# Kernel tuning notes

Hardware: AMD Instinct MI355X
Metric: run time of the kernel (lower is better)

## Reference

```python
import jax, jax.numpy as jnp
import numpy as np

N_NODES = 50000
N_EDGES = 800000
IN_DIM, HID, OUT_DIM = 32, 96, 1
NEG_SLOPE = 0.2


def _glorot(key, shape):
    fan_in, fan_out = shape[0], shape[-1]
    lim = float(np.sqrt(6.0 / (fan_in + fan_out)))
    return jax.random.uniform(key, shape, jnp.float32, -lim, lim)


def setup_inputs() -> dict:
    key = jax.random.key(0)
    ks = jax.random.split(key, 20)
    inp = {
        "x": jax.random.normal(ks[0], (N_NODES, IN_DIM), jnp.float32),
        "edge_index": jax.random.randint(ks[1], (2, N_EDGES), 0, N_NODES, jnp.int64),
        "edge_weight": jax.random.uniform(ks[2], (N_EDGES,), jnp.float32),
    }
    dims = [(IN_DIM, HID), (HID, HID), (HID, HID), (HID, OUT_DIM)]
    names = ["0", "1", "2", "f"]
    k = 3
    for nm, (di, do) in zip(names, dims):
        inp["W" + nm] = _glorot(ks[k], (di, do)); k += 1
        inp["as" + nm] = _glorot(ks[k], (1, do))[0]; k += 1
        inp["ad" + nm] = _glorot(ks[k], (1, do))[0]; k += 1
        inp["b" + nm] = jnp.zeros((do,), jnp.float32)
    return inp


def _gat_conv(x, src, dst, n, W, a_s, a_d, b):
    # h: [N, out]; per-node attention logits, gathered per edge
    h = x @ W
    es = h @ a_s  # [N]
    ed = h @ a_d  # [N]
    e = jax.nn.leaky_relu(es[src] + ed[dst], NEG_SLOPE)  # [E]
    m = jax.ops.segment_max(e, dst, num_segments=n)  # segment-softmax (stable)
    ex = jnp.exp(e - m[dst])
    s = jax.ops.segment_sum(ex, dst, num_segments=n)
    alpha = ex / s[dst]  # every node has a self loop -> s > 0
    out = jax.ops.segment_sum(alpha[:, None] * h[src], dst, num_segments=n)
    return out + b


def reference(x, edge_index, edge_weight, W0, as0, ad0, b0, W1, as1, ad1, b1,
              W2, as2, ad2, b2, Wf, asf, adf, bf):
    # edge_weight is ignored: PyG GATConv with edge_dim=None drops edge_attr.
    n = x.shape[0]
    loops = jnp.arange(n, dtype=edge_index.dtype)
    src = jnp.concatenate([edge_index[0], loops])  # add_self_loops=True
    dst = jnp.concatenate([edge_index[1], loops])

    # dropout is identity in eval mode
    for (W, a_s, a_d, b) in [(W0, as0, ad0, b0), (W1, as1, ad1, b1), (W2, as2, ad2, b2)]:
        residual = x
        x = _gat_conv(x, src, dst, n, W, a_s, a_d, b)
        if x.shape == residual.shape:
            x = x + residual
        x = jax.nn.relu(x)
    return _gat_conv(x, src, dst, n, Wf, asf, adf, bf)
```

## Files before the change

kernel.cpp:

```cpp
#include <hip/hip_runtime.h>
#include <hip/hip_fp16.h>
#include <math.h>

#define N_NODES 50000
#define N_EDGES 800000
#define E_TOT   (N_EDGES + N_NODES)
#define IN_DIM  32
#define HID     96
#define NEG_SLOPE 0.2f
#define BUCKET  48
#define G_PAD   50
#define NBINS   196
#define BCAP    5120
#define GC_STRIDE 64
#define FILL_EPT 16
#define FILL_NB ((N_EDGES + 256 * FILL_EPT - 1) / (256 * FILL_EPT))
#define AGG_BLOCKS (N_NODES / 16)
#define PREP_BLOCKS ((N_NODES * 32) / 256)
#define WT_BLOCKS (((HID * HID) + 255) / 256)

typedef _Float16 half8v __attribute__((ext_vector_type(8)));
typedef float    float4v __attribute__((ext_vector_type(4)));

static inline int cdiv(long long a, int b) { return (int)((a + b - 1) / b); }

__device__ __forceinline__ int clamp_src(int s) {
    return (int)min((unsigned)s, (unsigned)(N_NODES - 1));
}

__device__ __forceinline__ float lrelu_exp(float v) {
    v = v > 0.f ? v : NEG_SLOPE * v;
    return __expf(v);
}

__device__ __forceinline__ void mfma_tile_epilogue(
    const __half* s_x , __half* s_t ,
    const __half* __restrict__ wt, const float* __restrict__ a_s,
    const float* __restrict__ a_d, __half* __restrict__ h,
    float* __restrict__ es, float* __restrict__ ed, int m0, int lane) {
    int col = lane & 15, quad = lane >> 4;
    const __half* arow = s_x + col * 104 + quad * 8;
    const __half* brow = wt + (size_t)col * 96 + quad * 8;

    float ps0 = 0.f, ps1 = 0.f, ps2 = 0.f, ps3 = 0.f;
    float pd0 = 0.f, pd1 = 0.f, pd2 = 0.f, pd3 = 0.f;
    #pragma unroll
    for (int p = 0; p < 2; ++p) {
        float4v acc[3];
        #pragma unroll
        for (int t = 0; t < 3; ++t) acc[t] = (float4v){0.f, 0.f, 0.f, 0.f};
        #pragma unroll
        for (int ks = 0; ks < 3; ++ks) {
            half8v afrag = *(const half8v*)(arow + ks * 32);
            #pragma unroll
            for (int t = 0; t < 3; ++t) {
                half8v bfrag = *(const half8v*)(brow + (size_t)(p * 3 + t) * 16 * 96 + ks * 32);
                acc[t] = __builtin_amdgcn_mfma_f32_16x16x32_f16(afrag, bfrag, acc[t], 0, 0, 0);
            }
        }
        #pragma unroll
        for (int t = 0; t < 3; ++t) {
            int ch = (p * 3 + t) * 16 + col;
            float sa = a_s[ch], sd = a_d[ch];
            float v0 = acc[t][0], v1 = acc[t][1], v2 = acc[t][2], v3 = acc[t][3];
            int r0 = quad * 4;
            s_t[(r0 + 0) * 104 + ch] = __float2half(v0);
            s_t[(r0 + 1) * 104 + ch] = __float2half(v1);
            s_t[(r0 + 2) * 104 + ch] = __float2half(v2);
            s_t[(r0 + 3) * 104 + ch] = __float2half(v3);
            ps0 += v0 * sa; ps1 += v1 * sa; ps2 += v2 * sa; ps3 += v3 * sa;
            pd0 += v0 * sd; pd1 += v1 * sd; pd2 += v2 * sd; pd3 += v3 * sd;
        }
    }
    #pragma unroll
    for (int o = 1; o < 16; o <<= 1) {
        ps0 += __shfl_xor(ps0, o); ps1 += __shfl_xor(ps1, o);
        ps2 += __shfl_xor(ps2, o); ps3 += __shfl_xor(ps3, o);
        pd0 += __shfl_xor(pd0, o); pd1 += __shfl_xor(pd1, o);
        pd2 += __shfl_xor(pd2, o); pd3 += __shfl_xor(pd3, o);
    }
    if (col == 0) {
        int nb = m0 + quad * 4;
        es[nb] = ps0; es[nb + 1] = ps1; es[nb + 2] = ps2; es[nb + 3] = ps3;
        ed[nb] = pd0; ed[nb + 1] = pd1; ed[nb + 2] = pd2; ed[nb + 3] = pd3;
    }
    {
        int trow = lane >> 2, q = lane & 3;
        const uint4* sr = (const uint4*)(s_t + trow * 104);
        uint4* H8 = (uint4*)h;
        size_t rb = (size_t)(m0 + trow) * 12;
        H8[rb + q]     = sr[q];
        H8[rb + q + 4] = sr[q + 4];
        H8[rb + q + 8] = sr[q + 8];
    }
}

__global__ __launch_bounds__(256) void build_prep_kernel(
    const int* __restrict__ ei, unsigned* __restrict__ gcnt,
    unsigned* __restrict__ ebuf,
    const float* __restrict__ x, const float* __restrict__ W0,
    const float* __restrict__ as0, const float* __restrict__ ad0,
    __half* __restrict__ xh, float* __restrict__ es, float* __restrict__ ed,
    const float* __restrict__ W1, const float* __restrict__ W2,
    __half* __restrict__ WT1, __half* __restrict__ WT2) {
    int b = blockIdx.x;
    if (b < FILL_NB) {
        __shared__ unsigned lcnt[256];
        __shared__ unsigned lbase[256];
        int tid = threadIdx.x;
        lcnt[tid] = 0u;
        __syncthreads();
        int e0 = (b * 256 + tid) * FILL_EPT;
        bool val = e0 < N_EDGES;
        unsigned pk[FILL_EPT];
        unsigned short rank[FILL_EPT];
        if (val) {
            #pragma unroll
            for (int q = 0; q < FILL_EPT / 4; ++q) {
                int4 d4 = *(const int4*)(ei + N_EDGES + e0 + q * 4);
                int4 s4 = *(const int4*)(ei + e0 + q * 4);
                int dd[4] = {d4.x, d4.y, d4.z, d4.w};
                int ss[4] = {s4.x, s4.y, s4.z, s4.w};
                #pragma unroll
                for (int k = 0; k < 4; ++k) {
                    int d = clamp_src(dd[k]);
                    int bin = d >> 8;
                    pk[q * 4 + k] = (unsigned)clamp_src(ss[k]) | ((unsigned)(d & 255) << 16)
                                  | ((unsigned)bin << 24);
                    rank[q * 4 + k] = (unsigned short)atomicAdd(&lcnt[bin], 1u);
                }
            }
        }
        __syncthreads();
        if (tid < NBINS) {
            unsigned c = lcnt[tid];
            lbase[tid] = c ? atomicAdd(gcnt + (size_t)tid * GC_STRIDE, c) : 0u;
        }
        __syncthreads();
        if (val) {
            #pragma unroll
            for (int k = 0; k < FILL_EPT; ++k) {
                unsigned bin = pk[k] >> 24;
                unsigned pos = lbase[bin] + rank[k];
                if (pos < BCAP) ebuf[(size_t)bin * BCAP + pos] = pk[k];
            }
        }
        return;
    }
    b -= FILL_NB;
    if (b >= PREP_BLOCKS) {
        int i = (b - PREP_BLOCKS) * 256 + threadIdx.x;
        if (i < HID * HID) {
            int n = i / HID, k = i - n * HID;
            WT1[i] = __float2half(W1[k * HID + n]);
            WT2[i] = __float2half(W2[k * HID + n]);
        }
        return;
    }
    __shared__ float s_us[32], s_ud[32];
    if (threadIdx.x < 64) {
        int k = threadIdx.x & 31;
        int sel = threadIdx.x >> 5;
        const float* a = sel ? ad0 : as0;
        float acc = 0.f;
        #pragma unroll 8
        for (int c = 0; c < HID; ++c) acc += W0[k * HID + c] * a[c];
        if (sel) s_ud[k] = acc; else s_us[k] = acc;
    }
    __syncthreads();
    int idx = b * 256 + threadIdx.x;
    int node = idx >> 5;
    int k = threadIdx.x & 31;
    float xv = x[(size_t)node * 32 + k];
    float xnb = __shfl_xor(xv, 1);
    if ((k & 1) == 0) {
        __half2 h2v = __floats2half2_rn(xv, xnb);
        ((__half2*)xh)[((size_t)node * 32 + k) >> 1] = h2v;
    }
    float ps = xv * s_us[k], pd = xv * s_ud[k];
    #pragma unroll
    for (int o = 16; o; o >>= 1) {
        ps += __shfl_xor(ps, o);
        pd += __shfl_xor(pd, o);
    }
    if (k == 0) { es[node] = ps; ed[node] = pd; }
}

__global__ __launch_bounds__(256) void bucket_build_kernel(
    const unsigned* __restrict__ gcnt, const unsigned* __restrict__ ebuf,
    unsigned* __restrict__ cnt, unsigned short* __restrict__ srcs) {
    __shared__ unsigned short lsr[256][BUCKET];
    __shared__ unsigned lct[256];
    int bin = blockIdx.x, tid = threadIdx.x;
    int nb = bin * 256 + tid;
    lct[tid] = 1u;
    lsr[tid][0] = (unsigned short)min(nb, N_NODES - 1);
    __syncthreads();
    unsigned ec = min(gcnt[(size_t)bin * GC_STRIDE], (unsigned)BCAP);
    for (unsigned j = tid; j < ec; j += 256) {
        unsigned pkv = ebuf[(size_t)bin * BCAP + j];
        unsigned dloc = (pkv >> 16) & 255u;
        unsigned pos = atomicAdd(&lct[dloc], 1u);
        if (pos < BUCKET) lsr[dloc][pos] = (unsigned short)(pkv & 0xFFFFu);
    }
    __syncthreads();
    if (nb < N_NODES) cnt[nb] = min(lct[tid], (unsigned)BUCKET);
    const uint4* ls4 = (const uint4*)&lsr[0][0];
    uint4* gs4 = (uint4*)(srcs + (size_t)bin * 256 * BUCKET);
    for (int i = tid; i < 256 * (BUCKET / 8); i += 256) {
        int node = i / (BUCKET / 8);
        if (bin * 256 + node < N_NODES) gs4[i] = ls4[i];
    }
}

__global__ __launch_bounds__(256) void aggregate32_kernel(
    const unsigned* __restrict__ cnt, const unsigned short* __restrict__ srcs,
    const float* __restrict__ es, const float* __restrict__ ed,
    const __half* __restrict__ xh,
    const float* __restrict__ W0, const float* __restrict__ b0,
    __half* __restrict__ x16a,
    const __half* __restrict__ wt1, const float* __restrict__ as1,
    const float* __restrict__ ad1, __half* __restrict__ hA,
    float* __restrict__ es2, float* __restrict__ ed2) {
    __shared__ uint2 sh[4][4][G_PAD];
    __shared__ float s_ag[16][33];
    __shared__ float4 s_w0[32][24];
    __shared__ __align__(16) __half s_x[16 * 104];
    __shared__ __align__(16) __half s_t[16 * 104];
    const float4* W4g = (const float4*)W0;
    for (int i = threadIdx.x; i < 32 * 24; i += 256)
        s_w0[i / 24][i % 24] = W4g[i];

    int lane = threadIdx.x & 63;
    int wv = threadIdx.x >> 6;
    int g = lane >> 4, lin = lane & 15;
    int node = blockIdx.x * 16 + wv * 4 + g;
    size_t row = (size_t)node * BUCKET;
    int deg = min((int)cnt[node], BUCKET);
    float edv = ed[node];

    float lsum;
    {
        int jA = lin, jB = lin + 16, jC = lin + 32;
        bool bA = jA < deg, bB = jB < deg, bC = jC < deg;
        int sA = clamp_src((int)srcs[row + (bA ? jA : 0)]);
        int sB = clamp_src((int)srcs[row + (bB ? jB : 0)]);
        int sC = clamp_src((int)srcs[row + (bC ? jC : 0)]);
        float gA = es[sA], gB = es[sB], gC = es[sC];
        float eA = bA ? lrelu_exp(gA + edv) : 0.f;
        float eB = bB ? lrelu_exp(gB + edv) : 0.f;
        float eC = bC ? lrelu_exp(gC + edv) : 0.f;
        uint2 pA; pA.x = (unsigned)sA; pA.y = __float_as_uint(eA);
        uint2 pB; pB.x = (unsigned)sB; pB.y = __float_as_uint(eB);
        uint2 pC; pC.x = (unsigned)sC; pC.y = __float_as_uint(eC);
        if (bA) sh[wv][g][jA] = pA;
        if (bB) sh[wv][g][jB] = pB;
        if (bC) sh[wv][g][jC] = pC;
        lsum = eA + eB + eC;
    }
    float4 acc = {0.f, 0.f, 0.f, 0.f};
    const uint2* x2 = (const uint2*)xh;
    int h8sel = lin >> 3;
    int c = lin & 7;

    int j = 0;
    for (; j + 8 <= deg; j += 8) {
        uint2 p0 = sh[wv][g][j + h8sel];
        uint2 p1 = sh[wv][g][j + 2 + h8sel];
        uint2 p2 = sh[wv][g][j + 4 + h8sel];
        uint2 p3 = sh[wv][g][j + 6 + h8sel];
        uint2 q0 = x2[(size_t)p0.x * 8 + c];
        uint2 q1 = x2[(size_t)p1.x * 8 + c];
        uint2 q2 = x2[(size_t)p2.x * 8 + c];
        uint2 q3 = x2[(size_t)p3.x * 8 + c];
        float e0 = __uint_as_float(p0.y), e1 = __uint_as_float(p1.y);
        float e2 = __uint_as_float(p2.y), e3 = __uint_as_float(p3.y);
        float2 f00 = __half22float2(*(__half2*)&q0.x), f01 = __half22float2(*(__half2*)&q0.y);
        float2 f10 = __half22float2(*(__half2*)&q1.x), f11 = __half22float2(*(__half2*)&q1.y);
        float2 f20 = __half22float2(*(__half2*)&q2.x), f21 = __half22float2(*(__half2*)&q2.y);
        float2 f30 = __half22float2(*(__half2*)&q3.x), f31 = __half22float2(*(__half2*)&q3.y);
        acc.x += e0 * f00.x + e1 * f10.x + e2 * f20.x + e3 * f30.x;
        acc.y += e0 * f00.y + e1 * f10.y + e2 * f20.y + e3 * f30.y;
        acc.z += e0 * f01.x + e1 * f11.x + e2 * f21.x + e3 * f31.x;
        acc.w += e0 * f01.y + e1 * f11.y + e2 * f21.y + e3 * f31.y;
    }
    for (; j + 4 <= deg; j += 4) {
        uint2 p0 = sh[wv][g][j + h8sel];
        uint2 p1 = sh[wv][g][j + 2 + h8sel];
        uint2 q0 = x2[(size_t)p0.x * 8 + c];
        uint2 q1 = x2[(size_t)p1.x * 8 + c];
        float e0 = __uint_as_float(p0.y), e1 = __uint_as_float(p1.y);
        float2 f00 = __half22float2(*(__half2*)&q0.x), f01 = __half22float2(*(__half2*)&q0.y);
        float2 f10 = __half22float2(*(__half2*)&q1.x), f11 = __half22float2(*(__half2*)&q1.y);
        acc.x += e0 * f00.x + e1 * f10.x; acc.y += e0 * f00.y + e1 * f10.y;
        acc.z += e0 * f01.x + e1 * f11.x; acc.w += e0 * f01.y + e1 * f11.y;
    }
    for (; j < deg; j += 2) {
        int idx = j + h8sel;
        if (idx < deg) {
            uint2 p = sh[wv][g][idx];
            uint2 q = x2[(size_t)p.x * 8 + c];
            float e = __uint_as_float(p.y);
            float2 f0 = __half22float2(*(__half2*)&q.x);
            float2 f1 = __half22float2(*(__half2*)&q.y);
            acc.x += e * f0.x; acc.y += e * f0.y;
            acc.z += e * f1.x; acc.w += e * f1.y;
        }
    }
    #pragma unroll
    for (int o = 1; o < 16; o <<= 1) lsum += __shfl_xor(lsum, o);
    acc.x += __shfl_xor(acc.x, 8);
    acc.y += __shfl_xor(acc.y, 8);
    acc.z += __shfl_xor(acc.z, 8);
    acc.w += __shfl_xor(acc.w, 8);
    if (lin < 8) {
        float inv = 1.f / lsum;
        int n = wv * 4 + g;
        s_ag[n][lin * 4 + 0] = acc.x * inv;
        s_ag[n][lin * 4 + 1] = acc.y * inv;
        s_ag[n][lin * 4 + 2] = acc.z * inv;
        s_ag[n][lin * 4 + 3] = acc.w * inv;
    }
    __syncthreads();
    int t = threadIdx.x;
    if (t < 192) {
        int n = t / 12, c8 = t - n * 12;
        int onode = blockIdx.x * 16 + n;
        float4 a0v = {0.f, 0.f, 0.f, 0.f}, a1v = {0.f, 0.f, 0.f, 0.f};
        #pragma unroll 8
        for (int k = 0; k < 32; ++k) {
            float a = s_ag[n][k];
            float4 w0 = s_w0[k][c8 * 2], w1 = s_w0[k][c8 * 2 + 1];
            a0v.x += a * w0.x; a0v.y += a * w0.y; a0v.z += a * w0.z; a0v.w += a * w0.w;
            a1v.x += a * w1.x; a1v.y += a * w1.y; a1v.z += a * w1.z; a1v.w += a * w1.w;
        }
        float4 bb0 = ((const float4*)b0)[c8 * 2], bb1 = ((const float4*)b0)[c8 * 2 + 1];
        float v0 = fmaxf(a0v.x + bb0.x, 0.f), v1 = fmaxf(a0v.y + bb0.y, 0.f);
        float v2 = fmaxf(a0v.z + bb0.z, 0.f), v3 = fmaxf(a0v.w + bb0.w, 0.f);
        float v4 = fmaxf(a1v.x + bb1.x, 0.f), v5 = fmaxf(a1v.y + bb1.y, 0.f);
        float v6 = fmaxf(a1v.z + bb1.z, 0.f), v7 = fmaxf(a1v.w + bb1.w, 0.f);
        __half2 q0 = __floats2half2_rn(v0, v1), q1 = __floats2half2_rn(v2, v3);
        __half2 q2 = __floats2half2_rn(v4, v5), q3 = __floats2half2_rn(v6, v7);
        uint4 st; st.x = *(unsigned*)&q0; st.y = *(unsigned*)&q1;
        st.z = *(unsigned*)&q2; st.w = *(unsigned*)&q3;
        ((uint4*)x16a)[(size_t)onode * 12 + c8] = st;
        *(uint4*)(s_x + n * 104 + c8 * 8) = st;
    }
    __syncthreads();
    if (threadIdx.x < 64)
        mfma_tile_epilogue(s_x, s_t, wt1, as1, ad1, hA, es2, ed2,
                           blockIdx.x * 16, lane);
}

__global__ __launch_bounds__(256) void aggregate96_kernel(
    const unsigned* __restrict__ cnt, const unsigned short* __restrict__ srcs,
    const float* __restrict__ es, const float* __restrict__ ed,
    const __half* __restrict__ h, const float* __restrict__ b,
    const __half* __restrict__ res16, __half* __restrict__ out16,
    const float* __restrict__ Wf, float* __restrict__ hfin,
    const __half* __restrict__ wtproj, const float* __restrict__ as_n,
    const float* __restrict__ ad_n, __half* __restrict__ h_out,
    float* __restrict__ es_n, float* __restrict__ ed_n) {
    __shared__ uint2 sh[4][4][G_PAD];
    __shared__ __align__(16) __half s_x[16 * 104];
    __shared__ __align__(16) __half s_t[16 * 104];
    int lane = threadIdx.x & 63;
    int wv = threadIdx.x >> 6;
    int g = lane >> 4, lin = lane & 15;
    int node = blockIdx.x * 16 + wv * 4 + g;
    size_t row = (size_t)node * BUCKET;
    int deg = min((int)cnt[node], BUCKET);
    float edv = ed[node];

    float lsum;
    {
        int jA = lin, jB = lin + 16, jC = lin + 32;
        bool bA = jA < deg, bB = jB < deg, bC = jC < deg;
        int sA = clamp_src((int)srcs[row + (bA ? jA : 0)]);
        int sB = clamp_src((int)srcs[row + (bB ? jB : 0)]);
        int sC = clamp_src((int)srcs[row + (bC ? jC : 0)]);
        float gA = es[sA], gB = es[sB], gC = es[sC];
        float eA = bA ? lrelu_exp(gA + edv) : 0.f;
        float eB = bB ? lrelu_exp(gB + edv) : 0.f;
        float eC = bC ? lrelu_exp(gC + edv) : 0.f;
        uint2 pA; pA.x = (unsigned)sA; pA.y = __float_as_uint(eA);
        uint2 pB; pB.x = (unsigned)sB; pB.y = __float_as_uint(eB);
        uint2 pC; pC.x = (unsigned)sC; pC.y = __float_as_uint(eC);
        if (bA) sh[wv][g][jA] = pA;
        if (bB) sh[wv][g][jB] = pB;
        if (bC) sh[wv][g][jC] = pC;
        lsum = eA + eB + eC;
    }
    float a0 = 0.f, a1 = 0.f, a2 = 0.f, a3 = 0.f, a4 = 0.f, a5 = 0.f, a6 = 0.f, a7 = 0.f;
    const uint4* h8 = (const uint4*)h;
    bool act = (lin < 12);

    int j = 0;
    for (; j + 4 <= deg; j += 4) {
        uint2 p0 = sh[wv][g][j];
        uint2 p1 = sh[wv][g][j + 1];
        uint2 p2 = sh[wv][g][j + 2];
        uint2 p3 = sh[wv][g][j + 3];
        if (act) {
            uint4 q0 = h8[(size_t)p0.x * 12 + lin];
            uint4 q1 = h8[(size_t)p1.x * 12 + lin];
            uint4 q2 = h8[(size_t)p2.x * 12 + lin];
            uint4 q3 = h8[(size_t)p3.x * 12 + lin];
            float e0 = __uint_as_float(p0.y), e1 = __uint_as_float(p1.y);
            float e2 = __uint_as_float(p2.y), e3 = __uint_as_float(p3.y);
            float2 fa0 = __half22float2(*(__half2*)&q0.x), fa1 = __half22float2(*(__half2*)&q0.y);
            float2 fa2 = __half22float2(*(__half2*)&q0.z), fa3 = __half22float2(*(__half2*)&q0.w);
            float2 fb0 = __half22float2(*(__half2*)&q1.x), fb1 = __half22float2(*(__half2*)&q1.y);
            float2 fb2 = __half22float2(*(__half2*)&q1.z), fb3 = __half22float2(*(__half2*)&q1.w);
            float2 fc0 = __half22float2(*(__half2*)&q2.x), fc1 = __half22float2(*(__half2*)&q2.y);
            float2 fc2 = __half22float2(*(__half2*)&q2.z), fc3 = __half22float2(*(__half2*)&q2.w);
            float2 fd0 = __half22float2(*(__half2*)&q3.x), fd1 = __half22float2(*(__half2*)&q3.y);
            float2 fd2 = __half22float2(*(__half2*)&q3.z), fd3 = __half22float2(*(__half2*)&q3.w);
            a0 += e0 * fa0.x + e1 * fb0.x + e2 * fc0.x + e3 * fd0.x;
            a1 += e0 * fa0.y + e1 * fb0.y + e2 * fc0.y + e3 * fd0.y;
            a2 += e0 * fa1.x + e1 * fb1.x + e2 * fc1.x + e3 * fd1.x;
            a3 += e0 * fa1.y + e1 * fb1.y + e2 * fc1.y + e3 * fd1.y;
            a4 += e0 * fa2.x + e1 * fb2.x + e2 * fc2.x + e3 * fd2.x;
            a5 += e0 * fa2.y + e1 * fb2.y + e2 * fc2.y + e3 * fd2.y;
            a6 += e0 * fa3.x + e1 * fb3.x + e2 * fc3.x + e3 * fd3.x;
            a7 += e0 * fa3.y + e1 * fb3.y + e2 * fc3.y + e3 * fd3.y;
        }
    }
    for (; j < deg; ++j) {
        uint2 p = sh[wv][g][j];
        if (act) {
            uint4 q = h8[(size_t)p.x * 12 + lin];
            float e = __uint_as_float(p.y);
            float2 f0 = __half22float2(*(__half2*)&q.x);
            float2 f1 = __half22float2(*(__half2*)&q.y);
            float2 f2 = __half22float2(*(__half2*)&q.z);
            float2 f3 = __half22float2(*(__half2*)&q.w);
            a0 += e * f0.x; a1 += e * f0.y;
            a2 += e * f1.x; a3 += e * f1.y;
            a4 += e * f2.x; a5 += e * f2.y;
            a6 += e * f3.x; a7 += e * f3.y;
        }
    }
    #pragma unroll
    for (int o = 1; o < 16; o <<= 1) lsum += __shfl_xor(lsum, o);

    float pfin = 0.f;
    if (act) {
        float inv = 1.f / lsum;
        const float4* b4 = (const float4*)b;
        float4 bb0 = b4[lin * 2], bb1 = b4[lin * 2 + 1];
        float v0 = a0 * inv + bb0.x, v1 = a1 * inv + bb0.y;
        float v2 = a2 * inv + bb0.z, v3 = a3 * inv + bb0.w;
        float v4 = a4 * inv + bb1.x, v5 = a5 * inv + bb1.y;
        float v6 = a6 * inv + bb1.z, v7 = a7 * inv + bb1.w;
        if (res16) {
            uint4 rr = ((const uint4*)res16)[(size_t)node * 12 + lin];
            float2 r0 = __half22float2(*(__half2*)&rr.x);
            float2 r1 = __half22float2(*(__half2*)&rr.y);
            float2 r2 = __half22float2(*(__half2*)&rr.z);
            float2 r3 = __half22float2(*(__half2*)&rr.w);
            v0 += r0.x; v1 += r0.y; v2 += r1.x; v3 += r1.y;
            v4 += r2.x; v5 += r2.y; v6 += r3.x; v7 += r3.y;
        }
        v0 = fmaxf(v0, 0.f); v1 = fmaxf(v1, 0.f); v2 = fmaxf(v2, 0.f); v3 = fmaxf(v3, 0.f);
        v4 = fmaxf(v4, 0.f); v5 = fmaxf(v5, 0.f); v6 = fmaxf(v6, 0.f); v7 = fmaxf(v7, 0.f);
        __half2 q0 = __floats2half2_rn(v0, v1), q1 = __floats2half2_rn(v2, v3);
        __half2 q2 = __floats2half2_rn(v4, v5), q3 = __floats2half2_rn(v6, v7);
        uint4 st; st.x = *(unsigned*)&q0; st.y = *(unsigned*)&q1;
        st.z = *(unsigned*)&q2; st.w = *(unsigned*)&q3;
        if (out16) ((uint4*)out16)[(size_t)node * 12 + lin] = st;
        if (wtproj) {
            int n = wv * 4 + g;
            *(uint4*)(s_x + n * 104 + lin * 8) = st;
        }
        if (hfin) {
            const float4* w4 = (const float4*)Wf;
            float4 wf0 = w4[lin * 2], wf1 = w4[lin * 2 + 1];
            pfin = v0 * wf0.x + v1 * wf0.y + v2 * wf0.z + v3 * wf0.w
                 + v4 * wf1.x + v5 * wf1.y + v6 * wf1.z + v7 * wf1.w;
        }
    }
    if (hfin) {
        #pragma unroll
        for (int o = 1; o < 16; o <<= 1) pfin += __shfl_xor(pfin, o);
        if (lin == 0) hfin[node] = pfin;
    }
    if (wtproj) {
        __syncthreads();
        if (threadIdx.x < 64)
            mfma_tile_epilogue(s_x, s_t, wtproj, as_n, ad_n, h_out, es_n, ed_n,
                               blockIdx.x * 16, lane);
    }
}

__global__ __launch_bounds__(256) void aggregate1_kernel(
    const unsigned* __restrict__ cnt, const unsigned short* __restrict__ srcs,
    const float* __restrict__ hfin, const float* __restrict__ asf,
    const float* __restrict__ adf, const float* __restrict__ bf,
    float* __restrict__ out) {
    int lane = threadIdx.x & 63;
    int wv = threadIdx.x >> 6;
    int g = lane >> 4, lin = lane & 15;
    int node = blockIdx.x * 16 + wv * 4 + g;
    size_t row = (size_t)node * BUCKET;
    int deg = min((int)cnt[node], BUCKET);
    float as0 = asf[0], ad0 = adf[0];
    float edv = hfin[node] * ad0;

    float lsum = 0.f, acc = 0.f;
    for (int base = 0; base < deg; base += 32) {
        int i0 = base + lin * 2;
        if (i0 < deg) {
            unsigned sv = *(const unsigned*)(srcs + row + i0);
            int s0 = clamp_src((int)(sv & 0xFFFFu));
            int s1 = clamp_src((int)(sv >> 16));
            float h0 = hfin[s0], h1 = hfin[s1];
            float v0 = as0 * h0 + edv;
            v0 = v0 > 0.f ? v0 : NEG_SLOPE * v0;
            float ex0 = __expf(v0);
            lsum += ex0; acc += ex0 * h0;
            if (i0 + 1 < deg) {
                float v1 = as0 * h1 + edv;
                v1 = v1 > 0.f ? v1 : NEG_SLOPE * v1;
                float ex1 = __expf(v1);
                lsum += ex1; acc += ex1 * h1;
            }
        }
    }
    #pragma unroll
    for (int o = 1; o < 16; o <<= 1) {
        lsum += __shfl_xor(lsum, o);
        acc  += __shfl_xor(acc, o);
    }
    if (lin == 0) out[node] = acc / lsum + bf[0];
}


extern "C" void kernel_launch(void* const* d_in, const int* in_sizes, int n_in,
                              void* d_out, int out_size, void* d_ws, size_t ws_size,
                              hipStream_t stream) {
    const float* x  = (const float*)d_in[0];
    const int*   ei = (const int*)d_in[1];
    const float* W0 = (const float*)d_in[3];
    const float* as0 = (const float*)d_in[4];
    const float* ad0 = (const float*)d_in[5];
    const float* b0 = (const float*)d_in[6];
    const float* W1 = (const float*)d_in[7];
    const float* as1 = (const float*)d_in[8];
    const float* ad1 = (const float*)d_in[9];
    const float* b1 = (const float*)d_in[10];
    const float* W2 = (const float*)d_in[11];
    const float* as2 = (const float*)d_in[12];
    const float* ad2 = (const float*)d_in[13];
    const float* b2 = (const float*)d_in[14];
    const float* Wf = (const float*)d_in[15];
    const float* asf = (const float*)d_in[16];
    const float* adf = (const float*)d_in[17];
    const float* bf = (const float*)d_in[18];

    float* out = (float*)d_out;

    float* Hf = (float*)d_ws;
    __half* H16A = (__half*)Hf;
    __half* H16B = H16A + (size_t)N_NODES * HID;
    float* ES = Hf + (long long)N_NODES * HID;
    float* ED = ES + N_NODES;
    unsigned* CNT = (unsigned*)(ED + N_NODES);
    unsigned short* SRCS = (unsigned short*)(CNT + N_NODES);
    __half* X16A = (__half*)(SRCS + (size_t)N_NODES * BUCKET);
    __half* X16B = X16A + (size_t)N_NODES * HID;
    __half* WT1 = X16B + (size_t)N_NODES * HID;
    __half* WT2 = WT1 + HID * HID;
    float* HFIN = (float*)(WT2 + HID * HID);
    __half* XH = (__half*)(HFIN + N_NODES);
    unsigned* GCNT = (unsigned*)(XH + (size_t)N_NODES * 32);
    unsigned* EBUF = GCNT + (size_t)NBINS * GC_STRIDE;
    float* ES2 = (float*)(EBUF + (size_t)NBINS * BCAP);
    float* ED2 = ES2 + N_NODES;

    hipMemsetAsync(GCNT, 0, (size_t)NBINS * GC_STRIDE * sizeof(unsigned), stream);
    build_prep_kernel<<<FILL_NB + PREP_BLOCKS + WT_BLOCKS, 256, 0, stream>>>(
        ei, GCNT, EBUF, x, W0, as0, ad0, XH, ES, ED, W1, W2, WT1, WT2);
    bucket_build_kernel<<<NBINS, 256, 0, stream>>>(GCNT, EBUF, CNT, SRCS);

    aggregate32_kernel<<<AGG_BLOCKS, 256, 0, stream>>>(
        CNT, SRCS, ES, ED, XH, W0, b0, X16A, WT1, as1, ad1, H16A, ES2, ED2);

    aggregate96_kernel<<<AGG_BLOCKS, 256, 0, stream>>>(
        CNT, SRCS, ES2, ED2, H16A, b1, X16A, X16B, nullptr, nullptr,
        WT2, as2, ad2, H16B, ES, ED);

    aggregate96_kernel<<<AGG_BLOCKS, 256, 0, stream>>>(
        CNT, SRCS, ES, ED, H16B, b2, X16B, nullptr, Wf, HFIN,
        nullptr, nullptr, nullptr, nullptr, nullptr, nullptr);

    aggregate1_kernel<<<AGG_BLOCKS, 256, 0, stream>>>(CNT, SRCS, HFIN, asf, adf, bf, out);
}
```

Measured before the change: 231.7 us.

## Sort nodes by degree within bins to balance aggregation wavefronts

The bucket build now computes a per-bin counting sort of nodes by in-degree and writes a permutation array. All aggregation kernels process nodes in that permuted order, so each 16-lane group in a wavefront handles nodes of similar degree, which cuts divergence and idle lanes in the degree-bounded loops. The cost is an extra indirection per node, scattered writes of outputs, es/ed and h rows instead of contiguous ones, and a little more work in the bucket build kernel.

After: 242.7 us. 1.05x slower.

```diff
diff --git a/kernel.cpp b/kernel.cpp
--- a/kernel.cpp
+++ b/kernel.cpp
@@ -35,9 +35,10 @@
 
 __device__ __forceinline__ void mfma_tile_epilogue(
     const __half* s_x , __half* s_t ,
+    const int* s_perm ,
     const __half* __restrict__ wt, const float* __restrict__ a_s,
     const float* __restrict__ a_d, __half* __restrict__ h,
-    float* __restrict__ es, float* __restrict__ ed, int m0, int lane) {
+    float* __restrict__ es, float* __restrict__ ed, int lane) {
     int col = lane & 15, quad = lane >> 4;
     const __half* arow = s_x + col * 104 + quad * 8;
     const __half* brow = wt + (size_t)col * 96 + quad * 8;
@@ -80,15 +81,17 @@
         pd2 += __shfl_xor(pd2, o); pd3 += __shfl_xor(pd3, o);
     }
     if (col == 0) {
-        int nb = m0 + quad * 4;
-        es[nb] = ps0; es[nb + 1] = ps1; es[nb + 2] = ps2; es[nb + 3] = ps3;
-        ed[nb] = pd0; ed[nb + 1] = pd1; ed[nb + 2] = pd2; ed[nb + 3] = pd3;
+        int r0q = quad * 4;
+        es[s_perm[r0q + 0]] = ps0; es[s_perm[r0q + 1]] = ps1;
+        es[s_perm[r0q + 2]] = ps2; es[s_perm[r0q + 3]] = ps3;
+        ed[s_perm[r0q + 0]] = pd0; ed[s_perm[r0q + 1]] = pd1;
+        ed[s_perm[r0q + 2]] = pd2; ed[s_perm[r0q + 3]] = pd3;
     }
     {
         int trow = lane >> 2, q = lane & 3;
         const uint4* sr = (const uint4*)(s_t + trow * 104);
         uint4* H8 = (uint4*)h;
-        size_t rb = (size_t)(m0 + trow) * 12;
+        size_t rb = (size_t)s_perm[trow] * 12;
         H8[rb + q]     = sr[q];
         H8[rb + q + 4] = sr[q + 4];
         H8[rb + q + 8] = sr[q + 8];
@@ -188,13 +191,17 @@
 
 __global__ __launch_bounds__(256) void bucket_build_kernel(
     const unsigned* __restrict__ gcnt, const unsigned* __restrict__ ebuf,
-    unsigned* __restrict__ cnt, unsigned short* __restrict__ srcs) {
+    unsigned* __restrict__ cnt, unsigned short* __restrict__ srcs,
+    unsigned* __restrict__ perm) {
     __shared__ unsigned short lsr[256][BUCKET];
     __shared__ unsigned lct[256];
+    __shared__ unsigned hist[64];
+    __shared__ unsigned hbase[64];
     int bin = blockIdx.x, tid = threadIdx.x;
     int nb = bin * 256 + tid;
     lct[tid] = 1u;
     lsr[tid][0] = (unsigned short)min(nb, N_NODES - 1);
+    if (tid < 64) hist[tid] = 0u;
     __syncthreads();
     unsigned ec = min(gcnt[(size_t)bin * GC_STRIDE], (unsigned)BCAP);
     for (unsigned j = tid; j < ec; j += 256) {
@@ -204,16 +211,37 @@
         if (pos < BUCKET) lsr[dloc][pos] = (unsigned short)(pkv & 0xFFFFu);
     }
     __syncthreads();
-    if (nb < N_NODES) cnt[nb] = min(lct[tid], (unsigned)BUCKET);
+    int degn = -1;
+    if (nb < N_NODES) {
+        unsigned d = min(lct[tid], (unsigned)BUCKET);
+        cnt[nb] = d;
+        degn = (int)min(d, 63u);
+    }
     const uint4* ls4 = (const uint4*)&lsr[0][0];
     uint4* gs4 = (uint4*)(srcs + (size_t)bin * 256 * BUCKET);
     for (int i = tid; i < 256 * (BUCKET / 8); i += 256) {
         int node = i / (BUCKET / 8);
         if (bin * 256 + node < N_NODES) gs4[i] = ls4[i];
     }
+    unsigned rloc = 0;
+    if (degn >= 0) rloc = atomicAdd(&hist[degn], 1u);
+    __syncthreads();
+    if (tid < 64) {
+        unsigned v = hist[tid];
+        unsigned s = v;
+        #pragma unroll
+        for (int o = 1; o < 64; o <<= 1) {
+            unsigned t = __shfl_up(s, o);
+            if (tid >= o) s += t;
+        }
+        hbase[tid] = s - v;
+    }
+    __syncthreads();
+    if (degn >= 0) perm[bin * 256 + hbase[degn] + rloc] = (unsigned)nb;
 }
 
 __global__ __launch_bounds__(256) void aggregate32_kernel(
+    const unsigned* __restrict__ perm,
     const unsigned* __restrict__ cnt, const unsigned short* __restrict__ srcs,
     const float* __restrict__ es, const float* __restrict__ ed,
     const __half* __restrict__ xh,
@@ -227,14 +255,17 @@
     __shared__ float4 s_w0[32][24];
     __shared__ __align__(16) __half s_x[16 * 104];
     __shared__ __align__(16) __half s_t[16 * 104];
+    __shared__ int s_perm[16];
     const float4* W4g = (const float4*)W0;
     for (int i = threadIdx.x; i < 32 * 24; i += 256)
         s_w0[i / 24][i % 24] = W4g[i];
+    if (threadIdx.x < 16)
+        s_perm[threadIdx.x] = clamp_src((int)perm[blockIdx.x * 16 + threadIdx.x]);
 
     int lane = threadIdx.x & 63;
     int wv = threadIdx.x >> 6;
     int g = lane >> 4, lin = lane & 15;
-    int node = blockIdx.x * 16 + wv * 4 + g;
+    int node = clamp_src((int)perm[blockIdx.x * 16 + wv * 4 + g]);
     size_t row = (size_t)node * BUCKET;
     int deg = min((int)cnt[node], BUCKET);
     float edv = ed[node];
@@ -325,7 +356,7 @@
     int t = threadIdx.x;
     if (t < 192) {
         int n = t / 12, c8 = t - n * 12;
-        int onode = blockIdx.x * 16 + n;
+        int onode = s_perm[n];
         float4 a0v = {0.f, 0.f, 0.f, 0.f}, a1v = {0.f, 0.f, 0.f, 0.f};
         #pragma unroll 8
         for (int k = 0; k < 32; ++k) {
@@ -348,11 +379,11 @@
     }
     __syncthreads();
     if (threadIdx.x < 64)
-        mfma_tile_epilogue(s_x, s_t, wt1, as1, ad1, hA, es2, ed2,
-                           blockIdx.x * 16, lane);
+        mfma_tile_epilogue(s_x, s_t, s_perm, wt1, as1, ad1, hA, es2, ed2, lane);
 }
 
 __global__ __launch_bounds__(256) void aggregate96_kernel(
+    const unsigned* __restrict__ perm,
     const unsigned* __restrict__ cnt, const unsigned short* __restrict__ srcs,
     const float* __restrict__ es, const float* __restrict__ ed,
     const __half* __restrict__ h, const float* __restrict__ b,
@@ -364,10 +395,13 @@
     __shared__ uint2 sh[4][4][G_PAD];
     __shared__ __align__(16) __half s_x[16 * 104];
     __shared__ __align__(16) __half s_t[16 * 104];
+    __shared__ int s_perm[16];
+    if (threadIdx.x < 16)
+        s_perm[threadIdx.x] = clamp_src((int)perm[blockIdx.x * 16 + threadIdx.x]);
     int lane = threadIdx.x & 63;
     int wv = threadIdx.x >> 6;
     int g = lane >> 4, lin = lane & 15;
-    int node = blockIdx.x * 16 + wv * 4 + g;
+    int node = clamp_src((int)perm[blockIdx.x * 16 + wv * 4 + g]);
     size_t row = (size_t)node * BUCKET;
     int deg = min((int)cnt[node], BUCKET);
     float edv = ed[node];
@@ -488,12 +522,12 @@
     if (wtproj) {
         __syncthreads();
         if (threadIdx.x < 64)
-            mfma_tile_epilogue(s_x, s_t, wtproj, as_n, ad_n, h_out, es_n, ed_n,
-                               blockIdx.x * 16, lane);
+            mfma_tile_epilogue(s_x, s_t, s_perm, wtproj, as_n, ad_n, h_out, es_n, ed_n, lane);
     }
 }
 
 __global__ __launch_bounds__(256) void aggregate1_kernel(
+    const unsigned* __restrict__ perm,
     const unsigned* __restrict__ cnt, const unsigned short* __restrict__ srcs,
     const float* __restrict__ hfin, const float* __restrict__ asf,
     const float* __restrict__ adf, const float* __restrict__ bf,
@@ -501,7 +535,7 @@
     int lane = threadIdx.x & 63;
     int wv = threadIdx.x >> 6;
     int g = lane >> 4, lin = lane & 15;
-    int node = blockIdx.x * 16 + wv * 4 + g;
+    int node = clamp_src((int)perm[blockIdx.x * 16 + wv * 4 + g]);
     size_t row = (size_t)node * BUCKET;
     int deg = min((int)cnt[node], BUCKET);
     float as0 = asf[0], ad0 = adf[0];
@@ -577,22 +611,23 @@
     unsigned* EBUF = GCNT + (size_t)NBINS * GC_STRIDE;
     float* ES2 = (float*)(EBUF + (size_t)NBINS * BCAP);
     float* ED2 = ES2 + N_NODES;
+    unsigned* PERM = (unsigned*)(ED2 + N_NODES);
 
     hipMemsetAsync(GCNT, 0, (size_t)NBINS * GC_STRIDE * sizeof(unsigned), stream);
     build_prep_kernel<<<FILL_NB + PREP_BLOCKS + WT_BLOCKS, 256, 0, stream>>>(
         ei, GCNT, EBUF, x, W0, as0, ad0, XH, ES, ED, W1, W2, WT1, WT2);
-    bucket_build_kernel<<<NBINS, 256, 0, stream>>>(GCNT, EBUF, CNT, SRCS);
+    bucket_build_kernel<<<NBINS, 256, 0, stream>>>(GCNT, EBUF, CNT, SRCS, PERM);
 
     aggregate32_kernel<<<AGG_BLOCKS, 256, 0, stream>>>(
-        CNT, SRCS, ES, ED, XH, W0, b0, X16A, WT1, as1, ad1, H16A, ES2, ED2);
+        PERM, CNT, SRCS, ES, ED, XH, W0, b0, X16A, WT1, as1, ad1, H16A, ES2, ED2);
 
     aggregate96_kernel<<<AGG_BLOCKS, 256, 0, stream>>>(
-        CNT, SRCS, ES2, ED2, H16A, b1, X16A, X16B, nullptr, nullptr,
+        PERM, CNT, SRCS, ES2, ED2, H16A, b1, X16A, X16B, nullptr, nullptr,
         WT2, as2, ad2, H16B, ES, ED);
 
     aggregate96_kernel<<<AGG_BLOCKS, 256, 0, stream>>>(
-        CNT, SRCS, ES, ED, H16B, b2, X16B, nullptr, Wf, HFIN,
+        PERM, CNT, SRCS, ES, ED, H16B, b2, X16B, nullptr, Wf, HFIN,
         nullptr, nullptr, nullptr, nullptr, nullptr, nullptr);
 
-    aggregate1_kernel<<<AGG_BLOCKS, 256, 0, stream>>>(CNT, SRCS, HFIN, asf, adf, bf, out);
-}
+    aggregate1_kernel<<<AGG_BLOCKS, 256, 0, stream>>>(PERM, CNT, SRCS, HFIN, asf, adf, bf, out);
+}
```
